# Optimization experiments

Hardware: AMD Instinct MI355X
Metric: run time of the kernel (lower is better)

Reference implementation:

```python
import jax, jax.numpy as jnp
import numpy as np

NEG = -9e15
ALPHA = 0.2  # LeakyReLU negative slope


def setup_inputs() -> dict:
    key = jax.random.key(0)
    k1, k2, k3, k4, k5, k6 = jax.random.split(key, 6)
    N, Fin, Fout = 8192, 512, 64
    x = jax.random.normal(k1, (N, Fin), dtype=jnp.float32)
    adj = jax.random.randint(k2, (N, N), 0, 2, dtype=jnp.int32)
    W = jax.random.normal(k3, (Fin, Fout), dtype=jnp.float32) * 0.05
    b = jax.random.normal(k4, (Fout,), dtype=jnp.float32) * 0.05
    a = jax.random.normal(k5, (2 * Fout,), dtype=jnp.float32) * 0.05
    a_b = jax.random.normal(k6, (), dtype=jnp.float32) * 0.05
    return {"x": x, "adj": adj, "W": W, "b": b, "a": a, "a_b": a_b}


def reference(x, adj, W, b, a, a_b):
    Fout = W.shape[1]
    h = x @ W + b  # [N, Fout]
    # attn([h_i, h_j]) decomposes: e[i,j] = h_i . a_src + h_j . a_dst + a_b
    # (avoids materializing the [N, N, 2F] concat tensor; same math)
    s_src = h @ a[:Fout]  # [N]
    s_dst = h @ a[Fout:]  # [N]
    energy = s_src[:, None] + s_dst[None, :] + a_b  # [N, N]
    energy = jnp.where(energy > 0, energy, ALPHA * energy)  # LeakyReLU
    masked = jnp.where(adj > 0, energy, NEG)
    attn = jax.nn.softmax(masked, axis=-1)  # dropout p=0 in eval
    h_prime = attn @ h  # [N, Fout]
    return jax.nn.elu(h_prime)  # concat=True path
```

## Files before the change

kernel.cpp:

```cpp
#include <hip/hip_runtime.h>
#include <hip/hip_bf16.h>

#define N_NODES 8192
#define FIN 512
#define FOUT 64
#define LRELU_ALPHA 0.2f

typedef __attribute__((ext_vector_type(8))) short short8;
typedef __attribute__((ext_vector_type(4))) float floatx4;

__device__ __forceinline__ short f2bf_bits(float x) {
    __hip_bfloat16 h = __float2bfloat16(x);
    union { __hip_bfloat16 b; short s; } u; u.b = h; return u.s;
}

__device__ __forceinline__ float pval(float ssrc, float sd, int adjv) {
    float e = ssrc + sd;
    e = fmaxf(e, LRELU_ALPHA * e);
    float pv = __expf(e);
    return adjv > 0 ? pv : 0.0f;
}

__global__ __launch_bounds__(256) void gat_h(
    const float* __restrict__ x, const float* __restrict__ W,
    const float* __restrict__ bias, const float* __restrict__ a,
    const float* __restrict__ a_b,
    float* __restrict__ s_src, float* __restrict__ s_dst,
    unsigned short* __restrict__ hbfT)
{
    const int lane = threadIdx.x & 63;
    const int wave = threadIdx.x >> 6;
    const int r0 = (blockIdx.x * 4 + wave) * 4;

    float acc0 = 0.f, acc1 = 0.f, acc2 = 0.f, acc3 = 0.f;
    const float* x0 = x + (size_t)r0 * FIN;

    #pragma unroll 4
    for (int k = 0; k < FIN; k += 4) {
        float4 xa = *reinterpret_cast<const float4*>(x0 + k);
        float4 xb = *reinterpret_cast<const float4*>(x0 + FIN + k);
        float4 xc = *reinterpret_cast<const float4*>(x0 + 2 * FIN + k);
        float4 xd = *reinterpret_cast<const float4*>(x0 + 3 * FIN + k);
        float w0 = W[(k + 0) * FOUT + lane];
        float w1 = W[(k + 1) * FOUT + lane];
        float w2 = W[(k + 2) * FOUT + lane];
        float w3 = W[(k + 3) * FOUT + lane];
        acc0 = fmaf(xa.w, w3, fmaf(xa.z, w2, fmaf(xa.y, w1, fmaf(xa.x, w0, acc0))));
        acc1 = fmaf(xb.w, w3, fmaf(xb.z, w2, fmaf(xb.y, w1, fmaf(xb.x, w0, acc1))));
        acc2 = fmaf(xc.w, w3, fmaf(xc.z, w2, fmaf(xc.y, w1, fmaf(xc.x, w0, acc2))));
        acc3 = fmaf(xd.w, w3, fmaf(xd.z, w2, fmaf(xd.y, w1, fmaf(xd.x, w0, acc3))));
    }
    float bb = bias[lane];
    acc0 += bb; acc1 += bb; acc2 += bb; acc3 += bb;

    ushort4 pk;
    pk.x = (unsigned short)f2bf_bits(acc0);
    pk.y = (unsigned short)f2bf_bits(acc1);
    pk.z = (unsigned short)f2bf_bits(acc2);
    pk.w = (unsigned short)f2bf_bits(acc3);
    *reinterpret_cast<ushort4*>(hbfT + (size_t)lane * N_NODES + r0) = pk;

    float asrc = a[lane], adst = a[FOUT + lane];
    float ab = a_b[0];
    float ss0 = acc0 * asrc, ss1 = acc1 * asrc, ss2 = acc2 * asrc, ss3 = acc3 * asrc;
    float sd0 = acc0 * adst, sd1 = acc1 * adst, sd2 = acc2 * adst, sd3 = acc3 * adst;
    #pragma unroll
    for (int m = 32; m >= 1; m >>= 1) {
        ss0 += __shfl_xor(ss0, m); ss1 += __shfl_xor(ss1, m);
        ss2 += __shfl_xor(ss2, m); ss3 += __shfl_xor(ss3, m);
        sd0 += __shfl_xor(sd0, m); sd1 += __shfl_xor(sd1, m);
        sd2 += __shfl_xor(sd2, m); sd3 += __shfl_xor(sd3, m);
    }
    if (lane == 0) {
        float4 vs = { ss0 + ab, ss1 + ab, ss2 + ab, ss3 + ab };
        float4 vd = { sd0, sd1, sd2, sd3 };
        *reinterpret_cast<float4*>(s_src + r0) = vs;
        *reinterpret_cast<float4*>(s_dst + r0) = vd;
    }
}

__global__ __launch_bounds__(256) void gat_attn(
    const int* __restrict__ adj,
    const float* __restrict__ s_src,
    const float* __restrict__ s_dst,
    const unsigned short* __restrict__ hbfT,
    float* __restrict__ out)
{
    const int lane = threadIdx.x & 63;
    const int wave = threadIdx.x >> 6;
    const int i0 = blockIdx.x * 16;
    const int rowA = i0 + (lane & 15);
    const int ko = (lane >> 4) * 8;

    const float ssrc = s_src[rowA];
    floatx4 acc[4] = { {0.f,0.f,0.f,0.f},{0.f,0.f,0.f,0.f},
                       {0.f,0.f,0.f,0.f},{0.f,0.f,0.f,0.f} };
    float denom = 0.f;

    const size_t adjRow = (size_t)rowA * N_NODES;

    for (int jt = wave; jt < N_NODES / 64; jt += 4) {
        const int j0 = jt * 64;
        #pragma unroll
        for (int kk = 0; kk < 2; ++kk) {
            const int jb = j0 + kk * 32 + ko;
            int4 A0 = *reinterpret_cast<const int4*>(adj + adjRow + jb);
            int4 A1 = *reinterpret_cast<const int4*>(adj + adjRow + jb + 4);
            float4 S0 = *reinterpret_cast<const float4*>(s_dst + jb);
            float4 S1 = *reinterpret_cast<const float4*>(s_dst + jb + 4);
            float p0 = pval(ssrc, S0.x, A0.x);
            float p1 = pval(ssrc, S0.y, A0.y);
            float p2 = pval(ssrc, S0.z, A0.z);
            float p3 = pval(ssrc, S0.w, A0.w);
            float p4 = pval(ssrc, S1.x, A1.x);
            float p5 = pval(ssrc, S1.y, A1.y);
            float p6 = pval(ssrc, S1.z, A1.z);
            float p7 = pval(ssrc, S1.w, A1.w);
            denom += ((p0 + p1) + (p2 + p3)) + ((p4 + p5) + (p6 + p7));
            short8 af;
            af[0] = f2bf_bits(p0); af[1] = f2bf_bits(p1);
            af[2] = f2bf_bits(p2); af[3] = f2bf_bits(p3);
            af[4] = f2bf_bits(p4); af[5] = f2bf_bits(p5);
            af[6] = f2bf_bits(p6); af[7] = f2bf_bits(p7);
            #pragma unroll
            for (int n = 0; n < 4; ++n) {
                short8 bf = *reinterpret_cast<const short8*>(
                    hbfT + (size_t)(n * 16 + (lane & 15)) * N_NODES + jb);
                acc[n] = __builtin_amdgcn_mfma_f32_16x16x32_bf16(af, bf, acc[n], 0, 0, 0);
            }
        }
    }

    denom += __shfl_xor(denom, 16);
    denom += __shfl_xor(denom, 32);

    __shared__ floatx4 redbuf[4][4][64];
    __shared__ float dred[4][16];
    #pragma unroll
    for (int n = 0; n < 4; ++n) redbuf[wave][n][lane] = acc[n];
    if (lane < 16) dred[wave][lane] = denom;
    __syncthreads();

    floatx4 facc = redbuf[0][wave][lane];
    facc += redbuf[1][wave][lane];
    facc += redbuf[2][wave][lane];
    facc += redbuf[3][wave][lane];

    #pragma unroll
    for (int e = 0; e < 4; ++e) {
        const int r2 = (lane >> 4) * 4 + e;
        float dn = dred[0][r2] + dred[1][r2] + dred[2][r2] + dred[3][r2];
        float val = facc[e] / dn;
        val = val > 0.f ? val : (__expf(val) - 1.f);
        out[(size_t)(i0 + r2) * FOUT + wave * 16 + (lane & 15)] = val;
    }
}

extern "C" void kernel_launch(void* const* d_in, const int* in_sizes, int n_in,
                              void* d_out, int out_size, void* d_ws, size_t ws_size,
                              hipStream_t stream) {
    const float* x   = (const float*)d_in[0];
    const int*   adj = (const int*)d_in[1];
    const float* W   = (const float*)d_in[2];
    const float* b   = (const float*)d_in[3];
    const float* a   = (const float*)d_in[4];
    const float* a_b = (const float*)d_in[5];
    float* out = (float*)d_out;

    char* ws = (char*)d_ws;
    float* s_src = (float*)ws;
    float* s_dst = (float*)(ws + 32 * 1024);
    unsigned short* hbfT = (unsigned short*)(ws + 64 * 1024);

    hipLaunchKernelGGL(gat_h, dim3(N_NODES / 16), dim3(256), 0, stream,
                       x, W, b, a, a_b, s_src, s_dst, hbfT);
    hipLaunchKernelGGL(gat_attn, dim3(N_NODES / 16), dim3(256), 0, stream,
                       adj, s_src, s_dst, hbfT, out);
}
```

Before: 145.7 us.

## Stage adj tiles via async global-to-LDS double buffering and pre-swizzle h for MFMA

```diff
diff --git a/kernel.cpp b/kernel.cpp
--- a/kernel.cpp
+++ b/kernel.cpp
@@ -9,12 +9,11 @@
 typedef __attribute__((ext_vector_type(8))) short short8;
 typedef __attribute__((ext_vector_type(4))) float floatx4;
 
-__device__ __forceinline__ short f2bf_bits(float x) {
-    __hip_bfloat16 h = __float2bfloat16(x);
-    union { __hip_bfloat16 b; short s; } u; u.b = h; return u.s;
-}
-
-__device__ __forceinline__ float pval(float ssrc, float sd, int adjv) {
+static __device__ __forceinline__ short f2bf_bits(float x) {
+    union { __hip_bfloat16 b; short s; } u; u.b = __float2bfloat16(x); return u.s;
+}
+
+static __device__ __forceinline__ float pval(float ssrc, float sd, int adjv) {
     float e = ssrc + sd;
     e = fmaxf(e, LRELU_ALPHA * e);
     float pv = __expf(e);
@@ -26,7 +25,7 @@
     const float* __restrict__ bias, const float* __restrict__ a,
     const float* __restrict__ a_b,
     float* __restrict__ s_src, float* __restrict__ s_dst,
-    unsigned short* __restrict__ hbfT)
+    unsigned short* __restrict__ hswz)
 {
     const int lane = threadIdx.x & 63;
     const int wave = threadIdx.x >> 6;
@@ -53,12 +52,19 @@
     float bb = bias[lane];
     acc0 += bb; acc1 += bb; acc2 += bb; acc3 += bb;
 
-    ushort4 pk;
-    pk.x = (unsigned short)f2bf_bits(acc0);
-    pk.y = (unsigned short)f2bf_bits(acc1);
-    pk.z = (unsigned short)f2bf_bits(acc2);
-    pk.w = (unsigned short)f2bf_bits(acc3);
-    *reinterpret_cast<ushort4*>(hbfT + (size_t)lane * N_NODES + r0) = pk;
+    {
+        const int ks = r0 >> 5;
+        const int n = lane >> 4;
+        const int lane_dst = (lane & 15) + (((r0 >> 3) & 3) << 4);
+        const int e0 = r0 & 7;
+        ushort4 pk;
+        pk.x = (unsigned short)f2bf_bits(acc0);
+        pk.y = (unsigned short)f2bf_bits(acc1);
+        pk.z = (unsigned short)f2bf_bits(acc2);
+        pk.w = (unsigned short)f2bf_bits(acc3);
+        *reinterpret_cast<ushort4*>(
+            hswz + (size_t)((ks * 4 + n) * 64 + lane_dst) * 8 + e0) = pk;
+    }
 
     float asrc = a[lane], adst = a[FOUT + lane];
     float ab = a_b[0];
@@ -79,13 +85,31 @@
     }
 }
 
-__global__ __launch_bounds__(256) void gat_attn(
+static __device__ __forceinline__ void stage_tile(const int* __restrict__ adj,
+                                                  int i0, int j0, int lane,
+                                                  char* ldsbase) {
+    #pragma unroll
+    for (int t = 0; t < 4; ++t) {
+        const int r = t * 4 + (lane >> 4);
+        const int u = (lane & 15) * 4;
+        const int col = u ^ ((r & 7) << 2);
+        const int* g = adj + (size_t)(i0 + r) * N_NODES + j0 + col;
+        __builtin_amdgcn_global_load_lds(
+            (const __attribute__((address_space(1))) int*)g,
+            (__attribute__((address_space(3))) int*)(ldsbase + t * 1024),
+            16, 0, 0);
+    }
+}
+
+__global__ __launch_bounds__(512, 4) void gat_attn(
     const int* __restrict__ adj,
     const float* __restrict__ s_src,
     const float* __restrict__ s_dst,
-    const unsigned short* __restrict__ hbfT,
+    const unsigned short* __restrict__ hswz,
     float* __restrict__ out)
 {
+    __shared__ __align__(16) char smem[65536];
+
     const int lane = threadIdx.x & 63;
     const int wave = threadIdx.x >> 6;
     const int i0 = blockIdx.x * 16;
@@ -97,15 +121,31 @@
                        {0.f,0.f,0.f,0.f},{0.f,0.f,0.f,0.f} };
     float denom = 0.f;
 
-    const size_t adjRow = (size_t)rowA * N_NODES;
-
-    for (int jt = wave; jt < N_NODES / 64; jt += 4) {
+    char* buf0 = smem + wave * 8192;
+    char* buf1 = buf0 + 4096;
+
+    const int NT = (N_NODES / 64) / 8;
+    int jt = wave;
+    stage_tile(adj, i0, jt * 64, lane, buf0);
+
+    for (int t = 0; t < NT; ++t) {
+        const int* cur = (const int*)((t & 1) ? buf1 : buf0);
+        char* nxt = (t & 1) ? buf0 : buf1;
+
+        asm volatile("s_waitcnt vmcnt(0)" ::: "memory");
+        __builtin_amdgcn_sched_barrier(0);
+
+        if (t + 1 < NT) stage_tile(adj, i0, (jt + 8) * 64, lane, nxt);
+
         const int j0 = jt * 64;
+        const int r = lane & 15;
+        const int swz = (r & 7) << 2;
         #pragma unroll
         for (int kk = 0; kk < 2; ++kk) {
-            const int jb = j0 + kk * 32 + ko;
-            int4 A0 = *reinterpret_cast<const int4*>(adj + adjRow + jb);
-            int4 A1 = *reinterpret_cast<const int4*>(adj + adjRow + jb + 4);
+            const int c0 = kk * 32 + ko;
+            int4 A0 = *reinterpret_cast<const int4*>(cur + r * 64 + (c0 ^ swz));
+            int4 A1 = *reinterpret_cast<const int4*>(cur + r * 64 + ((c0 + 4) ^ swz));
+            const int jb = j0 + c0;
             float4 S0 = *reinterpret_cast<const float4*>(s_dst + jb);
             float4 S1 = *reinterpret_cast<const float4*>(s_dst + jb + 4);
             float p0 = pval(ssrc, S0.x, A0.x);
@@ -122,37 +162,42 @@
             af[2] = f2bf_bits(p2); af[3] = f2bf_bits(p3);
             af[4] = f2bf_bits(p4); af[5] = f2bf_bits(p5);
             af[6] = f2bf_bits(p6); af[7] = f2bf_bits(p7);
+            const int ks = jt * 2 + kk;
             #pragma unroll
             for (int n = 0; n < 4; ++n) {
                 short8 bf = *reinterpret_cast<const short8*>(
-                    hbfT + (size_t)(n * 16 + (lane & 15)) * N_NODES + jb);
+                    hswz + (size_t)((ks * 4 + n) * 64 + lane) * 8);
                 acc[n] = __builtin_amdgcn_mfma_f32_16x16x32_bf16(af, bf, acc[n], 0, 0, 0);
             }
         }
+        jt += 8;
     }
 
     denom += __shfl_xor(denom, 16);
     denom += __shfl_xor(denom, 32);
 
-    __shared__ floatx4 redbuf[4][4][64];
-    __shared__ float dred[4][16];
+    __syncthreads();
+    floatx4* redbuf = (floatx4*)smem;
+    float* dred = (float*)(smem + 32768);
     #pragma unroll
-    for (int n = 0; n < 4; ++n) redbuf[wave][n][lane] = acc[n];
-    if (lane < 16) dred[wave][lane] = denom;
+    for (int n = 0; n < 4; ++n) redbuf[(wave * 4 + n) * 64 + lane] = acc[n];
+    if (lane < 16) dred[wave * 16 + lane] = denom;
     __syncthreads();
 
-    floatx4 facc = redbuf[0][wave][lane];
-    facc += redbuf[1][wave][lane];
-    facc += redbuf[2][wave][lane];
-    facc += redbuf[3][wave][lane];
-
-    #pragma unroll
-    for (int e = 0; e < 4; ++e) {
-        const int r2 = (lane >> 4) * 4 + e;
-        float dn = dred[0][r2] + dred[1][r2] + dred[2][r2] + dred[3][r2];
-        float val = facc[e] / dn;
-        val = val > 0.f ? val : (__expf(val) - 1.f);
-        out[(size_t)(i0 + r2) * FOUT + wave * 16 + (lane & 15)] = val;
+    if (wave < 4) {
+        floatx4 facc = redbuf[wave * 64 + lane];
+        #pragma unroll
+        for (int v = 1; v < 8; ++v) facc += redbuf[(v * 4 + wave) * 64 + lane];
+        #pragma unroll
+        for (int e = 0; e < 4; ++e) {
+            const int r2 = (lane >> 4) * 4 + e;
+            float dn = 0.f;
+            #pragma unroll
+            for (int v = 0; v < 8; ++v) dn += dred[v * 16 + r2];
+            float val = facc[e] / dn;
+            val = val > 0.f ? val : (__expf(val) - 1.f);
+            out[(size_t)(i0 + r2) * FOUT + wave * 16 + (lane & 15)] = val;
+        }
     }
 }
 
@@ -170,10 +215,10 @@
     char* ws = (char*)d_ws;
     float* s_src = (float*)ws;
     float* s_dst = (float*)(ws + 32 * 1024);
-    unsigned short* hbfT = (unsigned short*)(ws + 64 * 1024);
+    unsigned short* hswz = (unsigned short*)(ws + 64 * 1024);
 
     hipLaunchKernelGGL(gat_h, dim3(N_NODES / 16), dim3(256), 0, stream,
-                       x, W, b, a, a_b, s_src, s_dst, hbfT);
-    hipLaunchKernelGGL(gat_attn, dim3(N_NODES / 16), dim3(256), 0, stream,
-                       adj, s_src, s_dst, hbfT, out);
-}
+                       x, W, b, a, a_b, s_src, s_dst, hswz);
+    hipLaunchKernelGGL(gat_attn, dim3(N_NODES / 16), dim3(512), 0, stream,
+                       adj, s_src, s_dst, hswz, out);
+}
```

Result: faster. 132.1 us (-9.4%).
